# Kernel tuning notes

Hardware: AMD Instinct MI355X
Metric: run time of the kernel (lower is better)

Reference implementation:

```python
import jax, jax.numpy as jnp
import numpy as np

B, EMB, P, K = 8192, 768, 96, 256
D = EMB // P  # dsub = 8


def setup_inputs() -> dict:
    key = jax.random.key(0)
    k1, k2 = jax.random.split(key)
    vecs = jax.random.normal(k1, (B, EMB), dtype=jnp.float32)
    # torch init: uniform(-1, 1)
    codebook = jax.random.uniform(k2, (P, K, D), dtype=jnp.float32, minval=-1.0, maxval=1.0)
    return {"vecs": vecs, "codebook": codebook}


def reference(vecs, codebook):
    b = vecs.shape[0]
    p, k, d = codebook.shape
    v = vecs.reshape(b, p, d)                                  # [B,P,D]
    # squared distances via expanded quadratic (avoids [B,P,K,D] broadcast):
    # ||v-c||^2 = ||v||^2 - 2 v.c + ||c||^2
    dots = jnp.einsum('bpd,pkd->bpk', v, codebook)             # [B,P,K]
    d2 = (jnp.sum(v * v, axis=-1, keepdims=True)               # [B,P,1]
          - 2.0 * dots
          + jnp.sum(codebook * codebook, axis=-1)[None])       # [1,P,K]
    proba = jax.nn.softmax(-d2, axis=-1)                       # [B,P,K]
    # straight-through hard assignment
    idx = jnp.argmax(proba, axis=-1)                           # [B,P]
    hard = jax.nn.one_hot(idx, k, dtype=proba.dtype)           # [B,P,K]
    ste = jax.lax.stop_gradient(hard - proba) + proba
    # reconstruct from codebook
    out = jnp.einsum('bpk,pkd->bpd', ste, codebook).reshape(b, p * d)
    return out
```

## Files before the change

### kernel.cpp

```cpp
#include <hip/hip_runtime.h>


typedef float f32x2 __attribute__((ext_vector_type(2)));
typedef float f32x4 __attribute__((ext_vector_type(4)));

#define TPB 256
#define KBQ 4
#define CHUNK 8

namespace {
constexpr int kB   = 8192;
constexpr int kEMB = 768;
constexpr int kP   = 96;
constexpr int kK   = 256;
constexpr int kD   = 8;
}

__device__ __forceinline__ f32x2 vfma2(f32x2 a, f32x2 b, f32x2 c) {
    f32x2 d;
    d.x = fmaf(a.x, b.x, c.x);
    d.y = fmaf(a.y, b.y, c.y);
    return d;
}

__device__ __forceinline__ float code_c2(const f32x2 c[4]) {
    f32x2 t = c[0] * c[0];
    t = vfma2(c[1], c[1], t);
    t = vfma2(c[2], c[2], t);
    t = vfma2(c[3], c[3], t);
    return t.x + t.y;
}

__device__ __forceinline__ float code_score(const f32x2 c[4], const f32x2 vs[4],
                                            float c2) {
    f32x2 a = vfma2(c[0], vs[0], f32x2{c2, 0.0f});
    a = vfma2(c[1], vs[1], a);
    a = vfma2(c[2], vs[2], a);
    a = vfma2(c[3], vs[3], a);
    return a.x + a.y;
}

__global__ __launch_bounds__(TPB, 3)
void pq_argmin_kernel(const float* __restrict__ vecs,
                      const float* __restrict__ codebook,
                      float* __restrict__ out)
{
    const int p = blockIdx.y;
    const int t = threadIdx.x;

    const float* __restrict__ cbp = codebook + (size_t)p * kK * kD;

    const int b0 = blockIdx.x * (TPB * KBQ) + t;
    f32x2 vs[KBQ][4];
#pragma unroll
    for (int q = 0; q < KBQ; ++q) {
        const f32x4* vp = reinterpret_cast<const f32x4*>(
            vecs + (size_t)(b0 + q * TPB) * kEMB + p * kD);
        f32x4 x = vp[0];
        f32x4 y = vp[1];
        vs[q][0] = f32x2{-2.0f * x.x, -2.0f * x.y};
        vs[q][1] = f32x2{-2.0f * x.z, -2.0f * x.w};
        vs[q][2] = f32x2{-2.0f * y.x, -2.0f * y.y};
        vs[q][3] = f32x2{-2.0f * y.z, -2.0f * y.w};
    }

    float best[KBQ];
    int   bch[KBQ];
#pragma unroll
    for (int q = 0; q < KBQ; ++q) {
        best[q] = __builtin_inff();
        bch[q] = 0;
    }

#pragma unroll 2
    for (int ch = 0; ch < kK / CHUNK; ++ch) {
        f32x2 cp[CHUNK][4];
        float c2[CHUNK];
#pragma unroll
        for (int c = 0; c < CHUNK; ++c) {
            const f32x2* cc = reinterpret_cast<const f32x2*>(
                cbp + (ch * CHUNK + c) * kD);
#pragma unroll
            for (int j = 0; j < 4; ++j) cp[c][j] = cc[j];
        }
#pragma unroll
        for (int c = 0; c < CHUNK; ++c) c2[c] = code_c2(cp[c]);

#pragma unroll
        for (int q = 0; q < KBQ; ++q) {
            float s0 = code_score(cp[0], vs[q], c2[0]);
            float s1 = code_score(cp[1], vs[q], c2[1]);
            float s2 = code_score(cp[2], vs[q], c2[2]);
            float s3 = code_score(cp[3], vs[q], c2[3]);
            float s4 = code_score(cp[4], vs[q], c2[4]);
            float s5 = code_score(cp[5], vs[q], c2[5]);
            float s6 = code_score(cp[6], vs[q], c2[6]);
            float s7 = code_score(cp[7], vs[q], c2[7]);
            float m1 = fminf(fminf(s0, s1), s2);
            float m2 = fminf(fminf(s3, s4), s5);
            float m3 = fminf(fminf(s6, s7), m1);
            float m  = fminf(m2, m3);
            if (m < best[q]) {
                best[q] = m;
                bch[q] = ch;
            }
        }
    }

#pragma unroll
    for (int q = 0; q < KBQ; ++q) {
        const int base = bch[q] * CHUNK;
        float s[CHUNK];
#pragma unroll
        for (int c = 0; c < CHUNK; ++c) {
            f32x2 cc[4];
            const f32x2* src = reinterpret_cast<const f32x2*>(
                cbp + (base + c) * kD);
#pragma unroll
            for (int j = 0; j < 4; ++j) cc[j] = src[j];
            s[c] = code_score(cc, vs[q], code_c2(cc));
        }
        int idx = base;
        bool fnd = (s[0] == best[q]);
#pragma unroll
        for (int c = 1; c < CHUNK; ++c) {
            bool e = (s[c] == best[q]) && !fnd;
            idx = e ? base + c : idx;
            fnd = fnd || (s[c] == best[q]);
        }
        const f32x4* row = reinterpret_cast<const f32x4*>(cbp + idx * kD);
        f32x4 r0 = row[0];
        f32x4 r1 = row[1];
        f32x4* op = reinterpret_cast<f32x4*>(
            out + (size_t)(b0 + q * TPB) * kEMB + p * kD);
        op[0] = r0;
        op[1] = r1;
    }
}

extern "C" void kernel_launch(void* const* d_in, const int* in_sizes, int n_in,
                              void* d_out, int out_size, void* d_ws, size_t ws_size,
                              hipStream_t stream)
{
    const float* vecs     = (const float*)d_in[0];
    const float* codebook = (const float*)d_in[1];
    float* out            = (float*)d_out;

    dim3 grid(kB / (TPB * KBQ), kP, 1);
    dim3 block(TPB, 1, 1);
    hipLaunchKernelGGL(pq_argmin_kernel, grid, block, 0, stream,
                       vecs, codebook, out);
}
```

Before: 142.2 us.

## Use packed FMA inline asm with scalar codebook operands and prefetch next chunk

Replaces the compiler's scalar FMAs with explicit v_pk_fma_f32 inline asm that takes the block-uniform codebook pair from SGPRs, so the codebook stays in scalar registers. It also adds software prefetching of the next codebook chunk, halves CHUNK to 4 and TPB to 128, and drops the unroll-2 pragma. The goal is to raise VALU throughput and hide scalar-load latency in the argmin loop. Risks: the 's' constraint forces the uniform loads into SGPRs, the smaller block changes grid occupancy, and c2 is now summed sequentially, which may reorder rounding against the rescore pass (both use the same c2_of, so they stay consistent).

```diff
diff --git a/kernel.cpp b/kernel.cpp
--- a/kernel.cpp
+++ b/kernel.cpp
@@ -4,9 +4,9 @@
 typedef float f32x2 __attribute__((ext_vector_type(2)));
 typedef float f32x4 __attribute__((ext_vector_type(4)));
 
-#define TPB 256
+#define TPB 128
 #define KBQ 4
-#define CHUNK 8
+#define CHUNK 4
 
 namespace {
 constexpr int kB   = 8192;
@@ -14,30 +14,59 @@
 constexpr int kP   = 96;
 constexpr int kK   = 256;
 constexpr int kD   = 8;
+constexpr int kNCH = kK / CHUNK;
 }
 
-__device__ __forceinline__ f32x2 vfma2(f32x2 a, f32x2 b, f32x2 c) {
+__device__ __forceinline__ f32x2 pk_fma_sv(f32x2 cs, f32x2 b, f32x2 acc) {
     f32x2 d;
-    d.x = fmaf(a.x, b.x, c.x);
-    d.y = fmaf(a.y, b.y, c.y);
+    asm("v_pk_fma_f32 %0, %1, %2, %3" : "=v"(d) : "s"(cs), "v"(b), "v"(acc));
+    return d;
+}
+__device__ __forceinline__ f32x2 pk_fma_vv(f32x2 a, f32x2 b, f32x2 acc) {
+    f32x2 d;
+    asm("v_pk_fma_f32 %0, %1, %2, %3" : "=v"(d) : "v"(a), "v"(b), "v"(acc));
     return d;
 }
 
-__device__ __forceinline__ float code_c2(const f32x2 c[4]) {
-    f32x2 t = c[0] * c[0];
-    t = vfma2(c[1], c[1], t);
-    t = vfma2(c[2], c[2], t);
-    t = vfma2(c[3], c[3], t);
-    return t.x + t.y;
+__device__ __forceinline__ float c2_of(f32x4 lo, f32x4 hi) {
+    float t = lo.x * lo.x;
+    t = fmaf(lo.y, lo.y, t);
+    t = fmaf(lo.z, lo.z, t);
+    t = fmaf(lo.w, lo.w, t);
+    t = fmaf(hi.x, hi.x, t);
+    t = fmaf(hi.y, hi.y, t);
+    t = fmaf(hi.z, hi.z, t);
+    t = fmaf(hi.w, hi.w, t);
+    return t;
 }
 
-__device__ __forceinline__ float code_score(const f32x2 c[4], const f32x2 vs[4],
-                                            float c2) {
-    f32x2 a = vfma2(c[0], vs[0], f32x2{c2, 0.0f});
-    a = vfma2(c[1], vs[1], a);
-    a = vfma2(c[2], vs[2], a);
-    a = vfma2(c[3], vs[3], a);
+__device__ __forceinline__ float score_s(f32x4 lo, f32x4 hi,
+                                         const f32x2 vs[4], f32x2 c2z) {
+    f32x2 a = pk_fma_sv(lo.xy, vs[0], c2z);
+    a = pk_fma_sv(lo.zw, vs[1], a);
+    a = pk_fma_sv(hi.xy, vs[2], a);
+    a = pk_fma_sv(hi.zw, vs[3], a);
     return a.x + a.y;
+}
+__device__ __forceinline__ float score_v(f32x4 lo, f32x4 hi,
+                                         const f32x2 vs[4], f32x2 c2z) {
+    f32x2 a = pk_fma_vv(lo.xy, vs[0], c2z);
+    a = pk_fma_vv(lo.zw, vs[1], a);
+    a = pk_fma_vv(hi.xy, vs[2], a);
+    a = pk_fma_vv(hi.zw, vs[3], a);
+    return a.x + a.y;
+}
+
+__device__ __forceinline__ void load_chunk(const float* __restrict__ cbp,
+                                           int ch, f32x4 lo[CHUNK],
+                                           f32x4 hi[CHUNK]) {
+#pragma unroll
+    for (int c = 0; c < CHUNK; ++c) {
+        const f32x4* pc = reinterpret_cast<const f32x4*>(
+            cbp + (ch * CHUNK + c) * kD);
+        lo[c] = pc[0];
+        hi[c] = pc[1];
+    }
 }
 
 __global__ __launch_bounds__(TPB, 3)
@@ -72,39 +101,36 @@
         bch[q] = 0;
     }
 
-#pragma unroll 2
-    for (int ch = 0; ch < kK / CHUNK; ++ch) {
-        f32x2 cp[CHUNK][4];
+    f32x4 lo[CHUNK], hi[CHUNK];
+    load_chunk(cbp, 0, lo, hi);
+
+    for (int ch = 0; ch < kNCH; ++ch) {
+        f32x4 nlo[CHUNK], nhi[CHUNK];
+        load_chunk(cbp, (ch + 1) & (kNCH - 1), nlo, nhi);
+
         float c2[CHUNK];
+        f32x2 c2z[CHUNK];
 #pragma unroll
         for (int c = 0; c < CHUNK; ++c) {
-            const f32x2* cc = reinterpret_cast<const f32x2*>(
-                cbp + (ch * CHUNK + c) * kD);
-#pragma unroll
-            for (int j = 0; j < 4; ++j) cp[c][j] = cc[j];
+            c2[c] = c2_of(lo[c], hi[c]);
+            c2z[c] = f32x2{c2[c], 0.0f};
         }
-#pragma unroll
-        for (int c = 0; c < CHUNK; ++c) c2[c] = code_c2(cp[c]);
 
 #pragma unroll
         for (int q = 0; q < KBQ; ++q) {
-            float s0 = code_score(cp[0], vs[q], c2[0]);
-            float s1 = code_score(cp[1], vs[q], c2[1]);
-            float s2 = code_score(cp[2], vs[q], c2[2]);
-            float s3 = code_score(cp[3], vs[q], c2[3]);
-            float s4 = code_score(cp[4], vs[q], c2[4]);
-            float s5 = code_score(cp[5], vs[q], c2[5]);
-            float s6 = code_score(cp[6], vs[q], c2[6]);
-            float s7 = code_score(cp[7], vs[q], c2[7]);
-            float m1 = fminf(fminf(s0, s1), s2);
-            float m2 = fminf(fminf(s3, s4), s5);
-            float m3 = fminf(fminf(s6, s7), m1);
-            float m  = fminf(m2, m3);
+            float s0 = score_s(lo[0], hi[0], vs[q], c2z[0]);
+            float s1 = score_s(lo[1], hi[1], vs[q], c2z[1]);
+            float s2 = score_s(lo[2], hi[2], vs[q], c2z[2]);
+            float s3 = score_s(lo[3], hi[3], vs[q], c2z[3]);
+            float m = fminf(fminf(fminf(s0, s1), s2), s3);
             if (m < best[q]) {
                 best[q] = m;
                 bch[q] = ch;
             }
         }
+
+#pragma unroll
+        for (int c = 0; c < CHUNK; ++c) { lo[c] = nlo[c]; hi[c] = nhi[c]; }
     }
 
 #pragma unroll
@@ -113,12 +139,12 @@
         float s[CHUNK];
 #pragma unroll
         for (int c = 0; c < CHUNK; ++c) {
-            f32x2 cc[4];
-            const f32x2* src = reinterpret_cast<const f32x2*>(
+            const f32x4* pc = reinterpret_cast<const f32x4*>(
                 cbp + (base + c) * kD);
-#pragma unroll
-            for (int j = 0; j < 4; ++j) cc[j] = src[j];
-            s[c] = code_score(cc, vs[q], code_c2(cc));
+            f32x4 clo = pc[0];
+            f32x4 chi = pc[1];
+            float cc2 = c2_of(clo, chi);
+            s[c] = score_v(clo, chi, vs[q], f32x2{cc2, 0.0f});
         }
         int idx = base;
         bool fnd = (s[0] == best[q]);
```

Result: no change. 143.1 us (+0.7%).
